# Performance work log

Measured on AMD Instinct MI355X. Metric: run time of the kernel, lower is better.

The kernel has to match this reference:

```python
import jax, jax.numpy as jnp
import numpy as np
from jax import lax

NUM_LAYERS = 16
KS = 31
H = W = 1024
N_PATCHES = 4


def setup_inputs() -> dict:
    key = jax.random.key(0)
    k1, k2, k3 = jax.random.split(key, 3)
    img = jax.random.normal(k1, (1, 3, H + KS - 1, W + KS - 1), dtype=jnp.float32)
    # depthwise blur kernels, normalized to sum to 1 per kernel (PSF-like)
    w = jax.random.uniform(k2, (3 * NUM_LAYERS, 1, KS, KS), dtype=jnp.float32)
    w = w / jnp.sum(w, axis=(2, 3), keepdims=True)
    alpha = jax.random.uniform(k3, (N_PATCHES, NUM_LAYERS, H, W), dtype=jnp.float32)
    return {"img": img, "idx": 2, "weights": w, "alpha_mattes": alpha}


def reference(img, idx, weights, alpha_mattes):
    B, C = img.shape[0], img.shape[1]
    # grouped depthwise conv: 3 groups, each input channel -> NUM_LAYERS outputs, VALID padding
    blurs = lax.conv_general_dilated(
        img, weights, window_strides=(1, 1), padding='VALID',
        dimension_numbers=('NCHW', 'OIHW', 'NCHW'), feature_group_count=C)
    Ho, Wo = blurs.shape[2], blurs.shape[3]
    blurs = blurs.reshape(B, C, NUM_LAYERS, Ho, Wo)          # (B, 3, L, H, W)
    alpha = alpha_mattes[idx].reshape(B, 1, NUM_LAYERS, Ho, Wo)  # (1, 1, L, H, W)
    blurry = jnp.sum(blurs * alpha, axis=2)                  # (B, 3, H, W)
    return blurry
```

## Files before the change

### kernel.cpp

```cpp
#include <hip/hip_runtime.h>
#include <stdint.h>


typedef short short8 __attribute__((ext_vector_type(8)));
typedef float f32x4 __attribute__((ext_vector_type(4)));
typedef uint32_t u32;
typedef u32 u32x4 __attribute__((ext_vector_type(4)));

#define W_IMG    1054
#define NKY      31
#define IMG_ROWS 38
#define IMG_ROWB 192
#define BOFF     (IMG_ROWS * IMG_ROWB)
#define B_BYTES  (NKY * 64 * 16)
#define LDS_BYTES (BOFF + B_BYTES)

__device__ __forceinline__ uint16_t f2bf(float f) {
    uint32_t u = __float_as_uint(f);
    uint32_t r = (u + 0x7fffu + ((u >> 16) & 1u)) >> 16;
    return (uint16_t)r;
}

__global__ __launch_bounds__(256, 4) void conv_fused(
    const float* __restrict__ img, const int* __restrict__ idxp,
    const float* __restrict__ wts, const float* __restrict__ alpha,
    float* __restrict__ out)
{
    __shared__ __align__(16) unsigned char sm[LDS_BYTES];

    const int tid = threadIdx.x;
    const int bid = blockIdx.x;
    const int bx = bid & 15;
    const int by = (bid >> 4) & 127;
    const int ch = bid >> 11;
    const int x0 = bx << 6;
    const int y0 = by << 3;

    const float* __restrict__ imgc = img + (size_t)ch * (W_IMG * W_IMG);
    const int idx = *idxp;

    for (int it = tid; it < IMG_ROWS * 24; it += 256) {
        int g4 = it % 24;
        int row = it / 24;
        int colbase = x0 + (g4 << 2);
        const float* gp = imgc + (size_t)(y0 + row) * W_IMG + colbase;
        uint64_t pack = 0;
        #pragma unroll
        for (int e = 0; e < 4; ++e) {
            int col = colbase + e;
            float f = (col < W_IMG) ? gp[e] : 0.0f;
            pack |= (uint64_t)f2bf(f) << (16 * e);
        }
        *(uint64_t*)(sm + row * IMG_ROWB + (g4 << 3)) = pack;
    }

    const float* __restrict__ wch = wts + (size_t)ch * 16 * 961;
    for (int it = tid; it < NKY * 64; it += 256) {
        int l = it & 63;
        int ky = it >> 6;
        int layer = l & 15;
        int h = l >> 4;
        union { uint16_t u[8]; short8 s; } pk;
        #pragma unroll
        for (int j = 0; j < 8; ++j) {
            int kx = (h << 3) + j;
            float f = (kx < 31) ? wch[layer * 961 + ky * 31 + kx] : 0.0f;
            pk.u[j] = f2bf(f);
        }
        *(short8*)(sm + BOFF + (it << 4)) = pk.s;
    }

    __syncthreads();

    const int lane = tid & 63;
    const int wv = tid >> 6;
    const int lj = lane & 15;
    const int hi = lane >> 4;
    const int ix = lane & 7;
    const int yp = (lane >> 3) & 1;
    const u32 abase = (u32)(2 * wv + yp) * IMG_ROWB + ((u32)(ix + hi) << 4);

    f32x4 acc[8];
    #pragma unroll
    for (int d = 0; d < 8; ++d) { f32x4 z = {0.f, 0.f, 0.f, 0.f}; acc[d] = z; }

    for (int ky = 0; ky < NKY; ++ky) {
        short8 bfrag = *(const short8*)(sm + BOFF + (((ky << 6) + lane) << 4));
        const unsigned char* ap0 = sm + abase + (u32)ky * IMG_ROWB;
        u32x4 lo = *(const u32x4*)(ap0);
        u32x4 hh = *(const u32x4*)(ap0 + 16);
        u32 l[8];
        #pragma unroll
        for (int i = 0; i < 4; ++i) { l[i] = lo[i]; l[i + 4] = hh[i]; }
        u32 a[7];
        #pragma unroll
        for (int i = 0; i < 7; ++i)
            a[i] = __builtin_amdgcn_alignbit(l[i + 1], l[i], 16);
        #pragma unroll
        for (int h = 0; h < 4; ++h) {
            union { u32 d[4]; short8 s; } fe, fo;
            #pragma unroll
            for (int i = 0; i < 4; ++i) { fe.d[i] = l[h + i]; fo.d[i] = a[h + i]; }
            acc[2 * h]     = __builtin_amdgcn_mfma_f32_16x16x32_bf16(fe.s, bfrag, acc[2 * h],     0, 0, 0);
            acc[2 * h + 1] = __builtin_amdgcn_mfma_f32_16x16x32_bf16(fo.s, bfrag, acc[2 * h + 1], 0, 0, 0);
        }
    }

    __syncthreads();
    float* bl = (float*)sm;

    #pragma unroll
    for (int d = 0; d < 8; ++d) {
        #pragma unroll
        for (int r = 0; r < 4; ++r) {
            int i = 4 * hi + r;
            int y = 2 * wv + (i >> 3);
            int x = d + ((i & 7) << 3);
            bl[(y * 64 + x) * 17 + lj] = acc[d][r];
        }
    }
    __syncthreads();

    const int r0 = tid >> 6;
    const int c0 = tid & 63;
    const float* __restrict__ al =
        alpha + (((size_t)idx * 16) << 20) + (size_t)y0 * 1024 + x0;
    float s0 = 0.f, s1 = 0.f;
    #pragma unroll
    for (int l = 0; l < 16; ++l) {
        const float* ap = al + ((size_t)l << 20);
        s0 += bl[tid * 17 + l]         * ap[r0 * 1024 + c0];
        s1 += bl[(tid + 256) * 17 + l] * ap[(r0 + 4) * 1024 + c0];
    }
    float* __restrict__ outc =
        out + ((size_t)ch << 20) + (size_t)y0 * 1024 + x0;
    outc[r0 * 1024 + c0] = s0;
    outc[(r0 + 4) * 1024 + c0] = s1;
}

extern "C" void kernel_launch(void* const* d_in, const int* in_sizes, int n_in,
                              void* d_out, int out_size, void* d_ws, size_t ws_size,
                              hipStream_t stream) {
    const float* img   = (const float*)d_in[0];
    const int*   idxp  = (const int*)d_in[1];
    const float* wts   = (const float*)d_in[2];
    const float* alpha = (const float*)d_in[3];
    float* out = (float*)d_out;

    conv_fused<<<dim3(3 * 128 * 16), dim3(256), 0, stream>>>(
        img, idxp, wts, alpha, out);
}
```

Before: 414.1 us.

## Double output tile height per block and prefetch weight fragments

Each block now computes 16 output rows instead of 8, with each wave running two row-pairs through the MFMA loop. This amortizes the image halo load and the per-block weight staging over twice the work, and halves the grid. The weight B-fragment for the next ky is loaded one iteration ahead to hide LDS latency. The epilogue writes the accumulators to LDS in two phases so the buffer size stays the same. The cost is twice the accumulator registers (64 floats), which may lower occupancy, plus fewer blocks to spread across CUs.

```diff
diff --git a/kernel.cpp b/kernel.cpp
--- a/kernel.cpp
+++ b/kernel.cpp
@@ -9,7 +9,8 @@
 
 #define W_IMG    1054
 #define NKY      31
-#define IMG_ROWS 38
+#define TILE_Y   16
+#define IMG_ROWS 46
 #define IMG_ROWB 192
 #define BOFF     (IMG_ROWS * IMG_ROWB)
 #define B_BYTES  (NKY * 64 * 16)
@@ -31,10 +32,10 @@
     const int tid = threadIdx.x;
     const int bid = blockIdx.x;
     const int bx = bid & 15;
-    const int by = (bid >> 4) & 127;
-    const int ch = bid >> 11;
+    const int by = (bid >> 4) & 63;
+    const int ch = bid >> 10;
     const int x0 = bx << 6;
-    const int y0 = by << 3;
+    const int y0 = by << 4;
 
     const float* __restrict__ imgc = img + (size_t)ch * (W_IMG * W_IMG);
     const int idx = *idxp;
@@ -78,64 +79,88 @@
     const int hi = lane >> 4;
     const int ix = lane & 7;
     const int yp = (lane >> 3) & 1;
-    const u32 abase = (u32)(2 * wv + yp) * IMG_ROWB + ((u32)(ix + hi) << 4);
+    const u32 abase0 = (u32)(4 * wv + yp) * IMG_ROWB + ((u32)(ix + hi) << 4);
+    const u32 abase1 = abase0 + 2 * IMG_ROWB;
+    const u32 bbase = BOFF + ((u32)lane << 4);
 
-    f32x4 acc[8];
+    f32x4 acc[16];
     #pragma unroll
-    for (int d = 0; d < 8; ++d) { f32x4 z = {0.f, 0.f, 0.f, 0.f}; acc[d] = z; }
+    for (int d = 0; d < 16; ++d) { f32x4 z = {0.f, 0.f, 0.f, 0.f}; acc[d] = z; }
 
+    short8 bfrag = *(const short8*)(sm + bbase);
     for (int ky = 0; ky < NKY; ++ky) {
-        short8 bfrag = *(const short8*)(sm + BOFF + (((ky << 6) + lane) << 4));
-        const unsigned char* ap0 = sm + abase + (u32)ky * IMG_ROWB;
-        u32x4 lo = *(const u32x4*)(ap0);
-        u32x4 hh = *(const u32x4*)(ap0 + 16);
-        u32 l[8];
+        const unsigned char* base = sm + (u32)ky * IMG_ROWB;
+        u32x4 lo0 = *(const u32x4*)(base + abase0);
+        u32x4 hh0 = *(const u32x4*)(base + abase0 + 16);
+        u32x4 lo1 = *(const u32x4*)(base + abase1);
+        u32x4 hh1 = *(const u32x4*)(base + abase1 + 16);
+        int kyn = (ky < NKY - 1) ? ky + 1 : ky;
+        short8 bnext = *(const short8*)(sm + bbase + ((u32)kyn << 10));
+
         #pragma unroll
-        for (int i = 0; i < 4; ++i) { l[i] = lo[i]; l[i + 4] = hh[i]; }
-        u32 a[7];
-        #pragma unroll
-        for (int i = 0; i < 7; ++i)
-            a[i] = __builtin_amdgcn_alignbit(l[i + 1], l[i], 16);
-        #pragma unroll
-        for (int h = 0; h < 4; ++h) {
-            union { u32 d[4]; short8 s; } fe, fo;
+        for (int rp = 0; rp < 2; ++rp) {
+            u32 l[8];
             #pragma unroll
-            for (int i = 0; i < 4; ++i) { fe.d[i] = l[h + i]; fo.d[i] = a[h + i]; }
-            acc[2 * h]     = __builtin_amdgcn_mfma_f32_16x16x32_bf16(fe.s, bfrag, acc[2 * h],     0, 0, 0);
-            acc[2 * h + 1] = __builtin_amdgcn_mfma_f32_16x16x32_bf16(fo.s, bfrag, acc[2 * h + 1], 0, 0, 0);
+            for (int i = 0; i < 4; ++i) {
+                l[i]     = rp ? lo1[i] : lo0[i];
+                l[i + 4] = rp ? hh1[i] : hh0[i];
+            }
+            u32 a[7];
+            #pragma unroll
+            for (int i = 0; i < 7; ++i)
+                a[i] = __builtin_amdgcn_alignbit(l[i + 1], l[i], 16);
+            #pragma unroll
+            for (int h = 0; h < 4; ++h) {
+                union { u32 d[4]; short8 s; } fe, fo;
+                #pragma unroll
+                for (int i = 0; i < 4; ++i) { fe.d[i] = l[h + i]; fo.d[i] = a[h + i]; }
+                acc[rp * 8 + 2 * h] =
+                    __builtin_amdgcn_mfma_f32_16x16x32_bf16(fe.s, bfrag, acc[rp * 8 + 2 * h], 0, 0, 0);
+                acc[rp * 8 + 2 * h + 1] =
+                    __builtin_amdgcn_mfma_f32_16x16x32_bf16(fo.s, bfrag, acc[rp * 8 + 2 * h + 1], 0, 0, 0);
+            }
         }
+        bfrag = bnext;
     }
 
-    __syncthreads();
     float* bl = (float*)sm;
-
-    #pragma unroll
-    for (int d = 0; d < 8; ++d) {
-        #pragma unroll
-        for (int r = 0; r < 4; ++r) {
-            int i = 4 * hi + r;
-            int y = 2 * wv + (i >> 3);
-            int x = d + ((i & 7) << 3);
-            bl[(y * 64 + x) * 17 + lj] = acc[d][r];
-        }
-    }
-    __syncthreads();
-
+    const float* __restrict__ al =
+        alpha + (((size_t)idx * 16) << 20) + (size_t)y0 * 1024 + x0;
+    float* __restrict__ outc =
+        out + ((size_t)ch << 20) + (size_t)y0 * 1024 + x0;
     const int r0 = tid >> 6;
     const int c0 = tid & 63;
-    const float* __restrict__ al =
-        alpha + (((size_t)idx * 16) << 20) + (size_t)y0 * 1024 + x0;
-    float s0 = 0.f, s1 = 0.f;
+
+    __syncthreads();
     #pragma unroll
-    for (int l = 0; l < 16; ++l) {
-        const float* ap = al + ((size_t)l << 20);
-        s0 += bl[tid * 17 + l]         * ap[r0 * 1024 + c0];
-        s1 += bl[(tid + 256) * 17 + l] * ap[(r0 + 4) * 1024 + c0];
+    for (int p = 0; p < 2; ++p) {
+        if ((wv >> 1) == p) {
+            #pragma unroll
+            for (int rp = 0; rp < 2; ++rp) {
+                #pragma unroll
+                for (int d = 0; d < 8; ++d) {
+                    #pragma unroll
+                    for (int r = 0; r < 4; ++r) {
+                        int i = 4 * hi + r;
+                        int yph = 4 * (wv & 1) + 2 * rp + (i >> 3);
+                        int x = d + ((i & 7) << 3);
+                        bl[(yph * 64 + x) * 17 + lj] = acc[rp * 8 + d][r];
+                    }
+                }
+            }
+        }
+        __syncthreads();
+        float s0 = 0.f, s1 = 0.f;
+        #pragma unroll
+        for (int l = 0; l < 16; ++l) {
+            const float* ap = al + ((size_t)l << 20);
+            s0 += bl[tid * 17 + l]         * ap[(size_t)(8 * p + r0) * 1024 + c0];
+            s1 += bl[(tid + 256) * 17 + l] * ap[(size_t)(8 * p + r0 + 4) * 1024 + c0];
+        }
+        outc[(size_t)(8 * p + r0) * 1024 + c0] = s0;
+        outc[(size_t)(8 * p + r0 + 4) * 1024 + c0] = s1;
+        if (p == 0) __syncthreads();
     }
-    float* __restrict__ outc =
-        out + ((size_t)ch << 20) + (size_t)y0 * 1024 + x0;
-    outc[r0 * 1024 + c0] = s0;
-    outc[(r0 + 4) * 1024 + c0] = s1;
 }
 
 extern "C" void kernel_launch(void* const* d_in, const int* in_sizes, int n_in,
@@ -147,6 +172,6 @@
     const float* alpha = (const float*)d_in[3];
     float* out = (float*)d_out;
 
-    conv_fused<<<dim3(3 * 128 * 16), dim3(256), 0, stream>>>(
+    conv_fused<<<dim3(3 * 64 * 16), dim3(256), 0, stream>>>(
         img, idxp, wts, alpha, out);
 }
```

After: 398.5 us. 1.04x faster.
